# Kernel optimization log

Measured on AMD Instinct MI355X. Metric: run time of the kernel, lower is better.

## Reference

```python
import jax, jax.numpy as jnp
import numpy as np

T, B, NN = 20, 4, 500            # timesteps, batch, nodes per sample
M = B * NN                        # big-batched node count = 2000
IN_D, H, H2, OUT = 2, 128, 64, 32


def setup_inputs() -> dict:
    key = jax.random.key(0)
    ks = jax.random.split(key, 16)
    positions = jax.random.normal(ks[0], (T, M, IN_D), jnp.float32)
    adjacency = (jax.random.uniform(ks[1], (T, M, M)) < 0.01).astype(jnp.float32)
    adjacency = adjacency * (1.0 - jnp.eye(M, dtype=jnp.float32))
    ego_mask = jax.random.bernoulli(ks[2], 0.8, (B, T, NN))
    s = lambda k, shp, fan: (jax.random.normal(k, shp, jnp.float32) / np.sqrt(fan)).astype(jnp.float32)
    return {
        'positions': positions,
        'adjacency': adjacency,
        'ego_mask': ego_mask,
        'W1': s(ks[3], (IN_D, H), IN_D), 'b1': jnp.zeros((H,), jnp.float32),
        'W2': s(ks[4], (H, H), H),       'b2': jnp.zeros((H,), jnp.float32),
        'W_ih': s(ks[5], (4 * H, H), H), 'W_hh': s(ks[6], (4 * H, H), H),
        'b_ih': jnp.zeros((4 * H,), jnp.float32), 'b_hh': jnp.zeros((4 * H,), jnp.float32),
        'fc1_w': s(ks[7], (H, H2), H),   'fc1_b': jnp.zeros((H2,), jnp.float32),
        'fc2_w': s(ks[8], (H2, OUT), H2), 'fc2_b': jnp.zeros((OUT,), jnp.float32),
    }


def _forward(positions, adjacency, ego_mask, W1, b1, W2, b2,
             W_ih, W_hh, b_ih, b_hh, fc1_w, fc1_b, fc2_w, fc2_b):
    # ego_mask [B,T,NN] -> [T, B*NN] (matches permute(1,0,2).reshape(T,-1))
    mask = jnp.transpose(ego_mask, (1, 0, 2)).reshape(T, M).astype(positions.dtype)

    def gcn_timestep(x_t, a_t, m_t):
        # masked subgraph + self loops on kept nodes (PyG GCNConv normalization)
        Ahat = a_t * m_t[:, None] * m_t[None, :] + jnp.diag(m_t)   # [M,M]
        deg = Ahat.sum(axis=0)                                      # in-degree (col sum)
        dinv = jnp.where(deg > 0, jax.lax.rsqrt(jnp.maximum(deg, 1e-12)), 0.0)
        An = dinv[:, None] * Ahat * dinv[None, :]                   # D^-1/2 Ahat D^-1/2
        h1 = jax.nn.relu(An.T @ (x_t @ W1) + b1)                    # GCN1 + relu
        h2 = (An.T @ (h1 @ W2) + b2) * m_t[:, None]                 # GCN2, scatter into zeros
        return h2

    placeholder = jax.vmap(gcn_timestep)(positions, adjacency, mask)  # [T, M, H]

    # torch nn.LSTM (batch_first=False) on placeholder.transpose(0,1):
    # sequence axis = nodes (M), batch axis = T
    xs = jnp.transpose(placeholder, (1, 0, 2))  # [M, T, H]

    def lstm_step(carry, x_s):
        h, c = carry
        gates = x_s @ W_ih.T + b_ih + h @ W_hh.T + b_hh
        i, f, g, o = jnp.split(gates, 4, axis=-1)
        c = jax.nn.sigmoid(f) * c + jax.nn.sigmoid(i) * jnp.tanh(g)
        h = jax.nn.sigmoid(o) * jnp.tanh(c)
        return (h, c), h

    init = (jnp.zeros((T, H), positions.dtype), jnp.zeros((T, H), positions.dtype))
    _, lstm_out = jax.lax.scan(lstm_step, init, xs)  # [M, T, H]

    emb = lstm_out.reshape(B, NN, T, H)              # view(B, max_nodes, T, H)
    emb = jax.nn.relu(emb @ fc1_w + fc1_b)
    return emb @ fc2_w + fc2_b                       # [B, NN, T, OUT]


def reference(positions, adjacency, ego_mask, W1, b1, W2, b2,
              W_ih, W_hh, b_ih, b_hh, fc1_w, fc1_b, fc2_w, fc2_b):
    return _forward(positions, adjacency, ego_mask, W1, b1, W2, b2,
                    W_ih, W_hh, b_ih, b_hh, fc1_w, fc1_b, fc2_w, fc2_b)
```

## Files before the change

kernel.cpp:

```cpp
#include <hip/hip_runtime.h>
#include <hip/hip_bf16.h>

#define T_   20
#define B_   4
#define NN_  500
#define M_   2000
#define TM_  40000
#define H_   128
#define G_   512
#define H2_  64
#define OUT_ 32
#define ECAP 64
#define TG_  (T_ * G_)

typedef unsigned short ushort_t;
typedef unsigned int   uint_t;
typedef _Float16       f16;
typedef f16 f16x2 __attribute__((ext_vector_type(2)));
typedef f16 f16x8 __attribute__((ext_vector_type(8)));
typedef float f32x4 __attribute__((ext_vector_type(4)));

#if defined(__has_builtin)
#  if __has_builtin(__builtin_amdgcn_fdot2)
#    define HAVE_FDOT2 1
#  endif
#endif

__device__ inline float fdot2_(f16x2 a, f16x2 b, float c) {
#ifdef HAVE_FDOT2
    return __builtin_amdgcn_fdot2(a, b, c, false);
#else
    return c + (float)a.x * (float)b.x + (float)a.y * (float)b.y;
#endif
}

__device__ inline float fast_sig(float x) {
    float e = __builtin_amdgcn_exp2f(x * -1.4426950408889634f);
    return __builtin_amdgcn_rcpf(1.f + e);
}
__device__ inline float fast_tanh(float x) {
    float e = __builtin_amdgcn_exp2f(x * 2.8853900817779268f);
    return 1.f - 2.f * __builtin_amdgcn_rcpf(e + 1.f);
}

#define BARRAW() asm volatile("s_barrier" ::: "memory")

__global__ __launch_bounds__(1024) void k0_mask(const void* __restrict__ ego,
                                                float* __restrict__ mf,
                                                int* __restrict__ ecnt) {
    __shared__ int fl[3];
    int tid = threadIdx.x;
    if (tid < 3) fl[tid] = 0;
    __syncthreads();
    const uint_t* dw = (const uint_t*)ego;
    int a = 0, b = 0, c = 0;
    for (int i = tid; i < 2500; i += 1024) {
        uint_t v = dw[i];
        bool isf32  = (v == 0x3F800000u);
        bool isbf16 = (v == 0x00003F80u) || (v == 0x3F803F80u);
        if (isf32)  a = 1;
        if (isbf16) b = 1;
        if (v > 1u && !isf32 && !isbf16) c = 1;
    }
    if (a) fl[0] = 1;
    if (b) fl[1] = 1;
    if (c) fl[2] = 1;
    __syncthreads();
    int mode;
    if (fl[1])      mode = 3;
    else if (fl[0]) mode = 2;
    else if (fl[2]) mode = 1;
    else            mode = 0;
    int e = blockIdx.x * 1024 + tid;
    if (e >= TM_) return;
    ecnt[e] = 0;
    int t = e / M_, i = e % M_;
    int bb = i / NN_, n = i % NN_;
    int src = (bb * T_ + t) * NN_ + n;
    bool on;
    if (mode == 0)      on = ((const int*)ego)[src] != 0;
    else if (mode == 1) on = ((const unsigned char*)ego)[src] != 0;
    else if (mode == 2) on = ((const float*)ego)[src] != 0.f;
    else                on = ((const ushort_t*)ego)[src] != 0;
    mf[e] = on ? 1.f : 0.f;
}

#define JSTRIP 200
__global__ void k1_scan(const float* __restrict__ adj, const float* __restrict__ mf,
                        int* __restrict__ ecnt, int* __restrict__ edges) {
    __shared__ float ms[JSTRIP];
    int t = blockIdx.y, j0 = blockIdx.z * JSTRIP;
    int i = blockIdx.x * 256 + threadIdx.x;
    for (int idx = threadIdx.x; idx < JSTRIP; idx += 256)
        ms[idx] = mf[t * M_ + j0 + idx];
    __syncthreads();
    if (i >= M_) return;
    if (mf[t * M_ + i] == 0.f) return;
    const float* ap = adj + (size_t)t * M_ * M_ + (size_t)j0 * M_ + i;
    int r = t * M_ + i;
    int* ep = edges + (size_t)r * ECAP;
#pragma unroll 8
    for (int jj = 0; jj < JSTRIP; ++jj) {
        float av = ap[(size_t)jj * M_];
        if (av != 0.f && ms[jj] != 0.f) {
            int pos = atomicAdd(&ecnt[r], 1);
            if (pos < ECAP) ep[pos] = j0 + jj;
        }
    }
}

__global__ void k2_y1(const float* __restrict__ pos, const float* __restrict__ W1,
                      const float* __restrict__ mf, const int* __restrict__ ecnt,
                      float* __restrict__ dinv, f16* __restrict__ Y1) {
    int gid = blockIdx.x * 256 + threadIdx.x;
    int r = gid >> 7, h = gid & 127;
    if (r >= TM_) return;
    float mr = mf[r];
    int cnt = ecnt[r];
    float dv = (mr != 0.f) ? __frsqrt_rn((float)(cnt + 1)) : 0.f;
    if (h == 0) dinv[r] = dv;
    float2 xy = ((const float2*)pos)[r];
    float v = xy.x * W1[h] + xy.y * W1[H_ + h];
    Y1[gid] = (f16)(dv * v);
}

__global__ __launch_bounds__(64) void k3_agg1(const f16* __restrict__ Y1,
        const float* __restrict__ dinv, const int* __restrict__ ecnt,
        const int* __restrict__ edges, const float* __restrict__ b1,
        f16* __restrict__ h1) {
    int r = blockIdx.x, q = threadIdx.x;
    int t = r / M_, base = t * M_;
    const uint_t* Yu = (const uint_t*)Y1;
    f16x2 sp = __builtin_bit_cast(f16x2, Yu[(size_t)r * 64 + q]);
    float a0 = (float)sp.x, a1 = (float)sp.y;
    int ec = ecnt[r]; if (ec > ECAP) ec = ECAP;
    const int4* ep4 = (const int4*)(edges + (size_t)r * ECAP);
    for (int e = 0; e < ec; e += 4) {
        int4 ix = ep4[e >> 2];
        int j1 = (e + 1 < ec) ? ix.y : ix.x;
        int j2 = (e + 2 < ec) ? ix.z : ix.x;
        int j3 = (e + 3 < ec) ? ix.w : ix.x;
        uint_t u0 = Yu[(size_t)(base + ix.x) * 64 + q];
        uint_t u1 = Yu[(size_t)(base + j1) * 64 + q];
        uint_t u2 = Yu[(size_t)(base + j2) * 64 + q];
        uint_t u3 = Yu[(size_t)(base + j3) * 64 + q];
        f16x2 p0 = __builtin_bit_cast(f16x2, u0);
        a0 += (float)p0.x; a1 += (float)p0.y;
        if (e + 1 < ec) { f16x2 p = __builtin_bit_cast(f16x2, u1); a0 += (float)p.x; a1 += (float)p.y; }
        if (e + 2 < ec) { f16x2 p = __builtin_bit_cast(f16x2, u2); a0 += (float)p.x; a1 += (float)p.y; }
        if (e + 3 < ec) { f16x2 p = __builtin_bit_cast(f16x2, u3); a0 += (float)p.x; a1 += (float)p.y; }
    }
    float dv = dinv[r];
    float o0 = dv * a0 + b1[2 * q];
    float o1 = dv * a1 + b1[2 * q + 1];
    f16x2 op; op.x = (f16)fmaxf(o0, 0.f); op.y = (f16)fmaxf(o1, 0.f);
    ((uint_t*)h1)[(size_t)r * 64 + q] = __builtin_bit_cast(uint_t, op);
}

__global__ __launch_bounds__(64) void k5_agg2(const f16* __restrict__ Y2,
        const float* __restrict__ dinv, const float* __restrict__ mf,
        const int* __restrict__ ecnt, const int* __restrict__ edges,
        const float* __restrict__ b2, f16* __restrict__ ph) {
    int r = blockIdx.x, q = threadIdx.x;
    int t = r / M_, base = t * M_;
    const uint_t* Yu = (const uint_t*)Y2;
    f16x2 sp = __builtin_bit_cast(f16x2, Yu[(size_t)r * 64 + q]);
    float a0 = (float)sp.x, a1 = (float)sp.y;
    int ec = ecnt[r]; if (ec > ECAP) ec = ECAP;
    const int4* ep4 = (const int4*)(edges + (size_t)r * ECAP);
    for (int e = 0; e < ec; e += 4) {
        int4 ix = ep4[e >> 2];
        int j1 = (e + 1 < ec) ? ix.y : ix.x;
        int j2 = (e + 2 < ec) ? ix.z : ix.x;
        int j3 = (e + 3 < ec) ? ix.w : ix.x;
        uint_t u0 = Yu[(size_t)(base + ix.x) * 64 + q];
        uint_t u1 = Yu[(size_t)(base + j1) * 64 + q];
        uint_t u2 = Yu[(size_t)(base + j2) * 64 + q];
        uint_t u3 = Yu[(size_t)(base + j3) * 64 + q];
        f16x2 p0 = __builtin_bit_cast(f16x2, u0);
        a0 += (float)p0.x; a1 += (float)p0.y;
        if (e + 1 < ec) { f16x2 p = __builtin_bit_cast(f16x2, u1); a0 += (float)p.x; a1 += (float)p.y; }
        if (e + 2 < ec) { f16x2 p = __builtin_bit_cast(f16x2, u2); a0 += (float)p.x; a1 += (float)p.y; }
        if (e + 3 < ec) { f16x2 p = __builtin_bit_cast(f16x2, u3); a0 += (float)p.x; a1 += (float)p.y; }
    }
    float dv = dinv[r], mr = mf[r];
    f16x2 op;
    op.x = (f16)((dv * a0 + b2[2 * q]) * mr);
    op.y = (f16)((dv * a1 + b2[2 * q + 1]) * mr);
    ((uint_t*)ph)[(size_t)r * 64 + q] = __builtin_bit_cast(uint_t, op);
}

#define ALD 136
__global__ __launch_bounds__(256) void kgemm_mfma(const f16* __restrict__ A,
        const float* __restrict__ Bw, int bTrans, int Ntot, int mode,
        const float* __restrict__ dinv, const float* __restrict__ ba,
        const float* __restrict__ bb, f16* __restrict__ Out) {
    __shared__ f16 As[64 * ALD];
    __shared__ f16 Bs[64 * ALD];
    int m0 = blockIdx.x * 64;
    int n0 = blockIdx.y * 64;
    int tid = threadIdx.x;
#pragma unroll
    for (int u = 0; u < 4; ++u) {
        int idx = u * 256 + tid;
        int row = idx >> 4, seg = idx & 15;
        *(f16x8*)&As[row * ALD + seg * 8] =
            *(const f16x8*)(A + (size_t)(m0 + row) * H_ + seg * 8);
    }
    if (bTrans) {
#pragma unroll
        for (int u = 0; u < 16; ++u) {
            int idx = u * 256 + tid;
            int n = idx >> 6, k2 = (idx & 63) * 2;
            float2 v = *(const float2*)(Bw + (size_t)(n0 + n) * H_ + k2);
            f16x2 pk; pk.x = (f16)v.x; pk.y = (f16)v.y;
            *(uint_t*)&Bs[n * ALD + k2] = __builtin_bit_cast(uint_t, pk);
        }
    } else {
#pragma unroll
        for (int u = 0; u < 16; ++u) {
            int idx = u * 256 + tid;
            int n = idx >> 6, k2 = (idx & 63) * 2;
            f16x2 pk;
            pk.x = (f16)Bw[(size_t)k2 * Ntot + n0 + n];
            pk.y = (f16)Bw[(size_t)(k2 + 1) * Ntot + n0 + n];
            *(uint_t*)&Bs[n * ALD + k2] = __builtin_bit_cast(uint_t, pk);
        }
    }
    __syncthreads();
    int w = tid >> 6, lane = tid & 63;
    int col = lane & 15, quad = lane >> 4;
    f32x4 acc[4] = {};
#pragma unroll
    for (int kk = 0; kk < 4; ++kk) {
        f16x8 af = *(const f16x8*)&As[(w * 16 + col) * ALD + kk * 32 + quad * 8];
#pragma unroll
        for (int nt = 0; nt < 4; ++nt) {
            f16x8 bf = *(const f16x8*)&Bs[(nt * 16 + col) * ALD + kk * 32 + quad * 8];
            acc[nt] = __builtin_amdgcn_mfma_f32_16x16x32_f16(af, bf, acc[nt], 0, 0, 0);
        }
    }
    if (mode == 0) {
        float dv[4];
#pragma unroll
        for (int reg = 0; reg < 4; ++reg)
            dv[reg] = dinv[m0 + w * 16 + quad * 4 + reg];
#pragma unroll
        for (int nt = 0; nt < 4; ++nt) {
            int n = n0 + nt * 16 + col;
#pragma unroll
            for (int reg = 0; reg < 4; ++reg) {
                int r = m0 + w * 16 + quad * 4 + reg;
                Out[(size_t)r * Ntot + n] = (f16)(dv[reg] * acc[nt][reg]);
            }
        }
    } else {
#pragma unroll
        for (int nt = 0; nt < 4; ++nt) {
            int n = n0 + nt * 16 + col;
            float bias = ba[n] + bb[n];
            int pos = (n & 127) * 4 + (n >> 7);
#pragma unroll
            for (int reg = 0; reg < 4; ++reg) {
                int r = m0 + w * 16 + quad * 4 + reg;
                int t = r / M_, s = r % M_;
                Out[((size_t)s * T_ + t) * G_ + pos] = (f16)(acc[nt][reg] + bias);
            }
        }
    }
}

__global__ __launch_bounds__(512, 2) void k7_lstm(const float* __restrict__ Whh,
        const f16* __restrict__ xg, f16* __restrict__ lo) {
    __shared__ ushort_t hb2[2][H_];
    int t = blockIdx.x, tid = threadIdx.x;
    int w = tid >> 6, lane = tid & 63;
    int col16 = lane & 15, quad = lane >> 4;
    int m = w * 16 + col16;
    f16x8 wf[4][4];
#pragma unroll
    for (int gt = 0; gt < 4; ++gt)
#pragma unroll
        for (int kk = 0; kk < 4; ++kk) {
            const float* wp = Whh + (size_t)(gt * H_ + m) * H_ + kk * 32 + quad * 8;
            float4 va = *(const float4*)wp;
            float4 vb = *(const float4*)(wp + 4);
            f16x8 f;
            f[0] = (f16)va.x; f[1] = (f16)va.y; f[2] = (f16)va.z; f[3] = (f16)va.w;
            f[4] = (f16)vb.x; f[5] = (f16)vb.y; f[6] = (f16)vb.z; f[7] = (f16)vb.w;
            wf[gt][kk] = f;
        }
    if (tid < H_) hb2[0][tid] = 0;
    float cst = 0.f;
    const f32x4 zero4 = {0.f, 0.f, 0.f, 0.f};
    const uint_t* xbase = (const uint_t*)xg;
    uint2 xa[4], xb[4];
    if (quad == 0) {
#pragma unroll
        for (int k = 0; k < 4; ++k)
            xa[k] = *(const uint2*)(xbase + ((size_t)k * T_ + t) * 256 + m * 2);
    }
    __syncthreads();

#define LSTM_STEP(S, XV)                                                      \
    do {                                                                      \
        const ushort_t* hp = &hb2[(S) & 1][0];                                \
        uint4 u0 = *(const uint4*)(hp + quad * 8);                            \
        uint4 u1 = *(const uint4*)(hp + 32 + quad * 8);                       \
        uint4 u2 = *(const uint4*)(hp + 64 + quad * 8);                       \
        uint4 u3 = *(const uint4*)(hp + 96 + quad * 8);                       \
        f16x8 a0 = __builtin_bit_cast(f16x8, u0);                             \
        f16x8 a1 = __builtin_bit_cast(f16x8, u1);                             \
        f16x8 a2 = __builtin_bit_cast(f16x8, u2);                             \
        f16x8 a3 = __builtin_bit_cast(f16x8, u3);                             \
        f32x4 g0 = __builtin_amdgcn_mfma_f32_16x16x32_f16(a0, wf[0][0], zero4, 0, 0, 0); \
        f32x4 g1 = __builtin_amdgcn_mfma_f32_16x16x32_f16(a0, wf[1][0], zero4, 0, 0, 0); \
        f32x4 g2 = __builtin_amdgcn_mfma_f32_16x16x32_f16(a0, wf[2][0], zero4, 0, 0, 0); \
        f32x4 g3 = __builtin_amdgcn_mfma_f32_16x16x32_f16(a0, wf[3][0], zero4, 0, 0, 0); \
        g0 = __builtin_amdgcn_mfma_f32_16x16x32_f16(a1, wf[0][1], g0, 0, 0, 0); \
        g1 = __builtin_amdgcn_mfma_f32_16x16x32_f16(a1, wf[1][1], g1, 0, 0, 0); \
        g2 = __builtin_amdgcn_mfma_f32_16x16x32_f16(a1, wf[2][1], g2, 0, 0, 0); \
        g3 = __builtin_amdgcn_mfma_f32_16x16x32_f16(a1, wf[3][1], g3, 0, 0, 0); \
        g0 = __builtin_amdgcn_mfma_f32_16x16x32_f16(a2, wf[0][2], g0, 0, 0, 0); \
        g1 = __builtin_amdgcn_mfma_f32_16x16x32_f16(a2, wf[1][2], g1, 0, 0, 0); \
        g2 = __builtin_amdgcn_mfma_f32_16x16x32_f16(a2, wf[2][2], g2, 0, 0, 0); \
        g3 = __builtin_amdgcn_mfma_f32_16x16x32_f16(a2, wf[3][2], g3, 0, 0, 0); \
        g0 = __builtin_amdgcn_mfma_f32_16x16x32_f16(a3, wf[0][3], g0, 0, 0, 0); \
        g1 = __builtin_amdgcn_mfma_f32_16x16x32_f16(a3, wf[1][3], g1, 0, 0, 0); \
        g2 = __builtin_amdgcn_mfma_f32_16x16x32_f16(a3, wf[2][3], g2, 0, 0, 0); \
        g3 = __builtin_amdgcn_mfma_f32_16x16x32_f16(a3, wf[3][3], g3, 0, 0, 0); \
        if (quad == 0) {                                                      \
            f16x2 xlo = __builtin_bit_cast(f16x2, (XV).x);                    \
            f16x2 xhi = __builtin_bit_cast(f16x2, (XV).y);                    \
            float gi = fast_sig(g0[0] + (float)xlo.x);                        \
            float gf = fast_sig(g1[0] + (float)xlo.y);                        \
            float gg = fast_tanh(g2[0] + (float)xhi.x);                       \
            float go = fast_sig(g3[0] + (float)xhi.y);                        \
            cst = gf * cst + gi * gg;                                         \
            float hv_ = go * fast_tanh(cst);                                  \
            f16 hh = (f16)hv_;                                                \
            hb2[((S) & 1) ^ 1][m] = __builtin_bit_cast(ushort_t, hh);         \
            lo[((size_t)(S) * T_ + t) * H_ + m] = hh;                         \
        }                                                                     \
        BARRAW();                                                             \
    } while (0)

    for (int c2 = 0; c2 < 250; ++c2) {
        int s0 = c2 * 8;
        if (quad == 0) {
#pragma unroll
            for (int k = 0; k < 4; ++k)
                xb[k] = *(const uint2*)(xbase + ((size_t)(s0 + 4 + k) * T_ + t) * 256 + m * 2);
        }
#pragma unroll
        for (int k = 0; k < 4; ++k) LSTM_STEP(s0 + k, xa[k]);
        int nbs = (s0 + 8 <= M_ - 4) ? s0 + 8 : M_ - 4;
        if (quad == 0) {
#pragma unroll
            for (int k = 0; k < 4; ++k)
                xa[k] = *(const uint2*)(xbase + ((size_t)(nbs + k) * T_ + t) * 256 + m * 2);
        }
#pragma unroll
        for (int k = 0; k < 4; ++k) LSTM_STEP(s0 + 4 + k, xb[k]);
    }
#undef LSTM_STEP
}

__global__ __launch_bounds__(256) void k8_fc(const f16* __restrict__ lo,
        const float* __restrict__ w1, const float* __restrict__ fb1,
        const float* __restrict__ w2, const float* __restrict__ fb2,
        float* __restrict__ out) {
    __shared__ uint_t hl[4][H_ / 2];
    __shared__ float o1f[4][H2_];
    int tid = threadIdx.x;
    int o = tid & 63, rr = tid >> 6;
    f16x2 w1c[64];
#pragma unroll
    for (int d = 0; d < 64; ++d) {
        f16x2 p;
        p.x = (f16)w1[(2 * d) * H2_ + o];
        p.y = (f16)w1[(2 * d + 1) * H2_ + o];
        w1c[d] = p;
    }
    int o2 = o & 31;
    float w2f[64];
#pragma unroll
    for (int d = 0; d < 64; ++d) w2f[d] = w2[d * OUT_ + o2];
    float fb1v = fb1[o], fb2v = fb2[o2];

    for (int r0 = blockIdx.x * 4; r0 < TM_; r0 += 512 * 4) {
        {
            int row = tid >> 6, qq = tid & 63;
            hl[row][qq] = ((const uint_t*)lo)[(size_t)(r0 + row) * 64 + qq];
        }
        __syncthreads();
        float acc = fb1v;
        const uint4* hb = (const uint4*)&hl[rr][0];
#pragma unroll
        for (int d = 0; d < 16; ++d) {
            uint4 hv = hb[d];
            acc = fdot2_(w1c[4 * d + 0], __builtin_bit_cast(f16x2, hv.x), acc);
            acc = fdot2_(w1c[4 * d + 1], __builtin_bit_cast(f16x2, hv.y), acc);
            acc = fdot2_(w1c[4 * d + 2], __builtin_bit_cast(f16x2, hv.z), acc);
            acc = fdot2_(w1c[4 * d + 3], __builtin_bit_cast(f16x2, hv.w), acc);
        }
        o1f[rr][o] = fmaxf(acc, 0.f);
        __syncthreads();
        if (o < OUT_) {
            float a2 = fb2v;
            const float4* ob = (const float4*)&o1f[rr][0];
#pragma unroll
            for (int d = 0; d < 16; ++d) {
                float4 v = ob[d];
                a2 += v.x * w2f[4 * d + 0] + v.y * w2f[4 * d + 1]
                    + v.z * w2f[4 * d + 2] + v.w * w2f[4 * d + 3];
            }
            out[(size_t)(r0 + rr) * OUT_ + o] = a2;
        }
        __syncthreads();
    }
}

extern "C" void kernel_launch(void* const* d_in, const int* in_sizes, int n_in,
                              void* d_out, int out_size, void* d_ws, size_t ws_size,
                              hipStream_t stream) {
    const float* positions = (const float*)d_in[0];
    const float* adjacency = (const float*)d_in[1];
    const void*  ego       = d_in[2];
    const float* W1   = (const float*)d_in[3];
    const float* b1   = (const float*)d_in[4];
    const float* W2   = (const float*)d_in[5];
    const float* b2   = (const float*)d_in[6];
    const float* W_ih = (const float*)d_in[7];
    const float* W_hh = (const float*)d_in[8];
    const float* b_ih = (const float*)d_in[9];
    const float* b_hh = (const float*)d_in[10];
    const float* fc1w = (const float*)d_in[11];
    const float* fc1b = (const float*)d_in[12];
    const float* fc2w = (const float*)d_in[13];
    const float* fc2b = (const float*)d_in[14];
    float* out = (float*)d_out;

    char* p = (char*)d_ws;
    auto alloc = [&](size_t bytes) {
        void* r = (void*)p;
        p += (bytes + 255) & ~(size_t)255;
        return r;
    };
    float* mf    = (float*)alloc((size_t)TM_ * 4);
    float* dinv  = (float*)alloc((size_t)TM_ * 4);
    int*   ecnt  = (int*)alloc((size_t)TM_ * 4);
    int*   edges = (int*)alloc((size_t)TM_ * ECAP * 4);
    f16*   bufC  = (f16*)alloc((size_t)TM_ * H_ * 2);
    f16*   bufD  = (f16*)alloc((size_t)TM_ * H_ * 2);
    f16*   xg    = (f16*)alloc((size_t)TM_ * G_ * 2);
    f16*   Y1 = bufC, *Y2 = bufC;
    f16*   h1 = bufD, *ph = bufD;
    f16*   lo = (f16*)edges;

    hipLaunchKernelGGL(k0_mask, dim3(40), dim3(1024), 0, stream, ego, mf, ecnt);
    hipLaunchKernelGGL(k1_scan, dim3(8, 20, 10), dim3(256), 0, stream,
                       adjacency, mf, ecnt, edges);
    hipLaunchKernelGGL(k2_y1, dim3(20000), dim3(256), 0, stream,
                       positions, W1, mf, ecnt, dinv, Y1);
    hipLaunchKernelGGL(k3_agg1, dim3(40000), dim3(64), 0, stream,
                       Y1, dinv, ecnt, edges, b1, h1);
    hipLaunchKernelGGL(kgemm_mfma, dim3(625, 2), dim3(256), 0, stream,
                       h1, W2, 0, 128, 0, dinv, (const float*)nullptr,
                       (const float*)nullptr, Y2);
    hipLaunchKernelGGL(k5_agg2, dim3(40000), dim3(64), 0, stream,
                       Y2, dinv, mf, ecnt, edges, b2, ph);
    hipLaunchKernelGGL(kgemm_mfma, dim3(625, 8), dim3(256), 0, stream,
                       ph, W_ih, 1, 512, 1, dinv, b_ih, b_hh, xg);
    hipLaunchKernelGGL(k7_lstm, dim3(20), dim3(512), 0, stream, W_hh, xg, lo);
    hipLaunchKernelGGL(k8_fc, dim3(512), dim3(256), 0, stream,
                       lo, fc1w, fc1b, fc2w, fc2b, out);
}
```

Before: 1.676 ms.

## Halve LSTM block to 4 waves, each wave computing 32 hidden units

```diff
diff --git a/kernel.cpp b/kernel.cpp
--- a/kernel.cpp
+++ b/kernel.cpp
@@ -270,35 +270,41 @@
     }
 }
 
-__global__ __launch_bounds__(512, 2) void k7_lstm(const float* __restrict__ Whh,
+__global__ __launch_bounds__(256, 1) void k7_lstm(const float* __restrict__ Whh,
         const f16* __restrict__ xg, f16* __restrict__ lo) {
     __shared__ ushort_t hb2[2][H_];
     int t = blockIdx.x, tid = threadIdx.x;
     int w = tid >> 6, lane = tid & 63;
     int col16 = lane & 15, quad = lane >> 4;
-    int m = w * 16 + col16;
-    f16x8 wf[4][4];
-#pragma unroll
-    for (int gt = 0; gt < 4; ++gt)
-#pragma unroll
-        for (int kk = 0; kk < 4; ++kk) {
-            const float* wp = Whh + (size_t)(gt * H_ + m) * H_ + kk * 32 + quad * 8;
-            float4 va = *(const float4*)wp;
-            float4 vb = *(const float4*)(wp + 4);
-            f16x8 f;
-            f[0] = (f16)va.x; f[1] = (f16)va.y; f[2] = (f16)va.z; f[3] = (f16)va.w;
-            f[4] = (f16)vb.x; f[5] = (f16)vb.y; f[6] = (f16)vb.z; f[7] = (f16)vb.w;
-            wf[gt][kk] = f;
-        }
+    f16x8 wf[2][4][4];
+#pragma unroll
+    for (int hb = 0; hb < 2; ++hb)
+#pragma unroll
+        for (int gt = 0; gt < 4; ++gt)
+#pragma unroll
+            for (int kk = 0; kk < 4; ++kk) {
+                const float* wp = Whh
+                    + (size_t)(gt * H_ + w * 32 + hb * 16 + col16) * H_
+                    + kk * 32 + quad * 8;
+                float4 va = *(const float4*)wp;
+                float4 vb = *(const float4*)(wp + 4);
+                f16x8 f;
+                f[0] = (f16)va.x; f[1] = (f16)va.y; f[2] = (f16)va.z; f[3] = (f16)va.w;
+                f[4] = (f16)vb.x; f[5] = (f16)vb.y; f[6] = (f16)vb.z; f[7] = (f16)vb.w;
+                wf[hb][gt][kk] = f;
+            }
     if (tid < H_) hb2[0][tid] = 0;
+    else          hb2[1][tid - H_] = 0;
+    bool upd = (quad < 2);
+    int midx = w * 32 + quad * 16 + col16;
     float cst = 0.f;
     const f32x4 zero4 = {0.f, 0.f, 0.f, 0.f};
     const uint_t* xbase = (const uint_t*)xg;
     uint2 xa[4], xb[4];
-    if (quad == 0) {
+    if (upd) {
 #pragma unroll
         for (int k = 0; k < 4; ++k)
-            xa[k] = *(const uint2*)(xbase + ((size_t)k * T_ + t) * 256 + m * 2);
+            xa[k] = *(const uint2*)(xbase + ((size_t)k * T_ + t) * 256 + midx * 2);
     }
     __syncthreads();
 
@@ -313,52 +319,53 @@
         f16x8 a1 = __builtin_bit_cast(f16x8, u1);                             \
         f16x8 a2 = __builtin_bit_cast(f16x8, u2);                             \
         f16x8 a3 = __builtin_bit_cast(f16x8, u3);                             \
-        f32x4 g0 = __builtin_amdgcn_mfma_f32_16x16x32_f16(a0, wf[0][0], zero4, 0, 0, 0); \
-        f32x4 g1 = __builtin_amdgcn_mfma_f32_16x16x32_f16(a0, wf[1][0], zero4, 0, 0, 0); \
-        f32x4 g2 = __builtin_amdgcn_mfma_f32_16x16x32_f16(a0, wf[2][0], zero4, 0, 0, 0); \
-        f32x4 g3 = __builtin_amdgcn_mfma_f32_16x16x32_f16(a0, wf[3][0], zero4, 0, 0, 0); \
-        g0 = __builtin_amdgcn_mfma_f32_16x16x32_f16(a1, wf[0][1], g0, 0, 0, 0); \
-        g1 = __builtin_amdgcn_mfma_f32_16x16x32_f16(a1, wf[1][1], g1, 0, 0, 0); \
-        g2 = __builtin_amdgcn_mfma_f32_16x16x32_f16(a1, wf[2][1], g2, 0, 0, 0); \
-        g3 = __builtin_amdgcn_mfma_f32_16x16x32_f16(a1, wf[3][1], g3, 0, 0, 0); \
-        g0 = __builtin_amdgcn_mfma_f32_16x16x32_f16(a2, wf[0][2], g0, 0, 0, 0); \
-        g1 = __builtin_amdgcn_mfma_f32_16x16x32_f16(a2, wf[1][2], g1, 0, 0, 0); \
-        g2 = __builtin_amdgcn_mfma_f32_16x16x32_f16(a2, wf[2][2], g2, 0, 0, 0); \
-        g3 = __builtin_amdgcn_mfma_f32_16x16x32_f16(a2, wf[3][2], g3, 0, 0, 0); \
-        g0 = __builtin_amdgcn_mfma_f32_16x16x32_f16(a3, wf[0][3], g0, 0, 0, 0); \
-        g1 = __builtin_amdgcn_mfma_f32_16x16x32_f16(a3, wf[1][3], g1, 0, 0, 0); \
-        g2 = __builtin_amdgcn_mfma_f32_16x16x32_f16(a3, wf[2][3], g2, 0, 0, 0); \
-        g3 = __builtin_amdgcn_mfma_f32_16x16x32_f16(a3, wf[3][3], g3, 0, 0, 0); \
-        if (quad == 0) {                                                      \
+        f32x4 acc[2][4];                                                      \
+        _Pragma("unroll")                                                     \
+        for (int hb = 0; hb < 2; ++hb) {                                      \
+            _Pragma("unroll")                                                 \
+            for (int gt = 0; gt < 4; ++gt) {                                  \
+                f32x4 g;                                                      \
+                g = __builtin_amdgcn_mfma_f32_16x16x32_f16(a0, wf[hb][gt][0], zero4, 0, 0, 0); \
+                g = __builtin_amdgcn_mfma_f32_16x16x32_f16(a1, wf[hb][gt][1], g, 0, 0, 0);     \
+                g = __builtin_amdgcn_mfma_f32_16x16x32_f16(a2, wf[hb][gt][2], g, 0, 0, 0);     \
+                g = __builtin_amdgcn_mfma_f32_16x16x32_f16(a3, wf[hb][gt][3], g, 0, 0, 0);     \
+                acc[hb][gt] = g;                                              \
+            }                                                                 \
+        }                                                                     \
+        if (upd) {                                                            \
+            float v0 = quad ? acc[1][0][0] : acc[0][0][0];                    \
+            float v1 = quad ? acc[1][1][0] : acc[0][1][0];                    \
+            float v2 = quad ? acc[1][2][0] : acc[0][2][0];                    \
+            float v3 = quad ? acc[1][3][0] : acc[0][3][0];                    \
             f16x2 xlo = __builtin_bit_cast(f16x2, (XV).x);                    \
             f16x2 xhi = __builtin_bit_cast(f16x2, (XV).y);                    \
-            float gi = fast_sig(g0[0] + (float)xlo.x);                        \
-            float gf = fast_sig(g1[0] + (float)xlo.y);                        \
-            float gg = fast_tanh(g2[0] + (float)xhi.x);                       \
-            float go = fast_sig(g3[0] + (float)xhi.y);                        \
+            float gi = fast_sig(v0 + (float)xlo.x);                           \
+            float gf = fast_sig(v1 + (float)xlo.y);                           \
+            float gg = fast_tanh(v2 + (float)xhi.x);                          \
+            float go = fast_sig(v3 + (float)xhi.y);                           \
             cst = gf * cst + gi * gg;                                         \
             float hv_ = go * fast_tanh(cst);                                  \
             f16 hh = (f16)hv_;                                                \
-            hb2[((S) & 1) ^ 1][m] = __builtin_bit_cast(ushort_t, hh);         \
-            lo[((size_t)(S) * T_ + t) * H_ + m] = hh;                         \
+            hb2[((S) & 1) ^ 1][midx] = __builtin_bit_cast(ushort_t, hh);      \
+            lo[((size_t)(S) * T_ + t) * H_ + midx] = hh;                      \
         }                                                                     \
         BARRAW();                                                             \
     } while (0)
 
     for (int c2 = 0; c2 < 250; ++c2) {
         int s0 = c2 * 8;
-        if (quad == 0) {
+        if (upd) {
 #pragma unroll
             for (int k = 0; k < 4; ++k)
-                xb[k] = *(const uint2*)(xbase + ((size_t)(s0 + 4 + k) * T_ + t) * 256 + m * 2);
+                xb[k] = *(const uint2*)(xbase + ((size_t)(s0 + 4 + k) * T_ + t) * 256 + midx * 2);
         }
 #pragma unroll
         for (int k = 0; k < 4; ++k) LSTM_STEP(s0 + k, xa[k]);
         int nbs = (s0 + 8 <= M_ - 4) ? s0 + 8 : M_ - 4;
-        if (quad == 0) {
+        if (upd) {
 #pragma unroll
             for (int k = 0; k < 4; ++k)
-                xa[k] = *(const uint2*)(xbase + ((size_t)(nbs + k) * T_ + t) * 256 + m * 2);
+                xa[k] = *(const uint2*)(xbase + ((size_t)(nbs + k) * T_ + t) * 256 + midx * 2);
         }
 #pragma unroll
         for (int k = 0; k < 4; ++k) LSTM_STEP(s0 + 4 + k, xb[k]);
@@ -472,7 +479,7 @@
                        Y2, dinv, mf, ecnt, edges, b2, ph);
     hipLaunchKernelGGL(kgemm_mfma, dim3(625, 8), dim3(256), 0, stream,
                        ph, W_ih, 1, 512, 1, dinv, b_ih, b_hh, xg);
-    hipLaunchKernelGGL(k7_lstm, dim3(20), dim3(512), 0, stream, W_hh, xg, lo);
+    hipLaunchKernelGGL(k7_lstm, dim3(20), dim3(256), 0, stream, W_hh, xg, lo);
     hipLaunchKernelGGL(k8_fc, dim3(512), dim3(256), 0, stream,
                        lo, fc1w, fc1b, fc2w, fc2b, out);
 }
```

New measurement: 1.654 ms. About the same (-1.4%).
